# Performance work log

Measured on AMD Instinct MI355X. Metric: run time of the kernel, lower is better.

Reference implementation:

```python
import jax, jax.numpy as jnp
import numpy as np

S, B, D, H, F, E = 2048, 2, 768, 12, 3072, 8
DH = D // H
T = S * B
CAP = int(2.0 * T / E)  # capacity factor 2.0


def layer_norm(x, g, b, eps=1e-5):
    m = jnp.mean(x, axis=-1, keepdims=True)
    v = jnp.var(x, axis=-1, keepdims=True)
    return (x - m) * jax.lax.rsqrt(v + eps) * g + b


def setup_inputs() -> dict:
    key = jax.random.key(0)
    ks = jax.random.split(key, 16)
    sc = 0.02
    return {
        "src": jax.random.normal(ks[0], (S, B, D), jnp.float32),
        "in_proj_w": sc * jax.random.normal(ks[1], (3 * D, D), jnp.float32),
        "in_proj_b": sc * jax.random.normal(ks[2], (3 * D,), jnp.float32),
        "out_proj_w": sc * jax.random.normal(ks[3], (D, D), jnp.float32),
        "out_proj_b": sc * jax.random.normal(ks[4], (D,), jnp.float32),
        "norm1_g": 1.0 + sc * jax.random.normal(ks[5], (D,), jnp.float32),
        "norm1_b": sc * jax.random.normal(ks[6], (D,), jnp.float32),
        "router_w": sc * jax.random.normal(ks[7], (E, D), jnp.float32),
        "router_b": sc * jax.random.normal(ks[8], (E,), jnp.float32),
        "w1": sc * jax.random.normal(ks[9], (E, D, F), jnp.float32),
        "b1": sc * jax.random.normal(ks[10], (E, F), jnp.float32),
        "w2": sc * jax.random.normal(ks[11], (E, F, D), jnp.float32),
        "b2": sc * jax.random.normal(ks[12], (E, D), jnp.float32),
        "norm2_g": 1.0 + sc * jax.random.normal(ks[13], (D,), jnp.float32),
        "norm2_b": sc * jax.random.normal(ks[14], (D,), jnp.float32),
    }


def reference(src, in_proj_w, in_proj_b, out_proj_w, out_proj_b,
              norm1_g, norm1_b, router_w, router_b, w1, b1, w2, b2,
              norm2_g, norm2_b):
    # ---- multi-head self-attention (dropout = identity, eval mode) ----
    qkv = src @ in_proj_w.T + in_proj_b                # [S,B,3D]
    q, k, v = jnp.split(qkv, 3, axis=-1)

    def heads(t):  # [S,B,D] -> [B,H,S,DH]
        return t.reshape(S, B, H, DH).transpose(1, 2, 0, 3)

    q, k, v = heads(q), heads(k), heads(v)
    scores = jnp.einsum('bhsd,bhtd->bhst', q, k) / np.float32(np.sqrt(DH))
    attn = jax.nn.softmax(scores, axis=-1)
    ctx = jnp.einsum('bhst,bhtd->bhsd', attn, v)       # [B,H,S,DH]
    ctx = ctx.transpose(2, 0, 1, 3).reshape(S, B, D)
    attn_out = ctx @ out_proj_w.T + out_proj_b

    x = layer_norm(src + attn_out, norm1_g, norm1_b)

    # ---- Switch MoE FFN: top-1 routing, capacity-based dispatch ----
    tok = x.reshape(T, D)
    logits = tok @ router_w.T + router_b               # [T,E]
    probs = jax.nn.softmax(logits, axis=-1)
    eidx = jnp.argmax(probs, axis=-1)                  # [T]
    gate = jnp.take_along_axis(probs, eidx[:, None], axis=-1)[:, 0]
    oh = jax.nn.one_hot(eidx, E, dtype=probs.dtype)    # [T,E]
    # position of each token within its expert's queue
    pos = (jnp.cumsum(oh, axis=0) * oh).sum(-1).astype(jnp.int32) - 1

    # scatter tokens into per-expert buffers (tokens over capacity dropped)
    buf = jnp.zeros((E, CAP, D), tok.dtype).at[eidx, pos].set(tok, mode='drop')
    h = jax.nn.relu(jnp.einsum('ecd,edf->ecf', buf, w1) + b1[:, None, :])
    y = jnp.einsum('ecf,efd->ecd', h, w2) + b2[:, None, :]

    keep = pos < CAP
    out_tok = jnp.where(keep[:, None], y[eidx, jnp.minimum(pos, CAP - 1)], 0.0)
    out_tok = out_tok * gate[:, None]
    moe_out = out_tok.reshape(S, B, D)

    # load-balancing loss: E * sum_e(frac_tokens_e * mean_prob_e)
    f = oh.mean(axis=0)
    P = probs.mean(axis=0)
    lb_loss = E * jnp.sum(f * P)

    out = layer_norm(x + moe_out, norm2_g, norm2_b)
    return (out, lb_loss)
```

## Files before the change

kernel.cpp:

```cpp
#include <hip/hip_runtime.h>
#include <hip/hip_bf16.h>


#define S_   2048
#define B_   2
#define D_   768
#define H_   12
#define DH_  64
#define F_   3072
#define E_   8
#define T_   4096
#define CAP_ 1024

typedef __hip_bfloat16 bf16;
using short8  = __attribute__((ext_vector_type(8))) short;
using floatx4 = __attribute__((ext_vector_type(4))) float;

__device__ __forceinline__ float b2f(bf16 x) { return __bfloat162float(x); }
__device__ __forceinline__ bf16  f2b(float x) { return __float2bfloat16(x); }

struct SrcF32 { const float* p; };
struct SrcPair { const bf16* h; const bf16* l; };

__device__ __forceinline__ void ld_split(const SrcF32& s, size_t off,
                                         short8& hi, short8& lo) {
  const float* q = s.p + off;
  float4 a = *(const float4*)q;
  float4 b = *(const float4*)(q + 4);
  float va[8] = {a.x, a.y, a.z, a.w, b.x, b.y, b.z, b.w};
  __attribute__((aligned(16))) bf16 h[8], l[8];
#pragma unroll
  for (int j = 0; j < 8; j++) {
    bf16 hh = f2b(va[j]);
    h[j] = hh;
    l[j] = f2b(va[j] - b2f(hh));
  }
  hi = *(const short8*)h; lo = *(const short8*)l;
}
__device__ __forceinline__ void ld_split(const SrcPair& s, size_t off,
                                         short8& hi, short8& lo) {
  hi = *(const short8*)(s.h + off);
  lo = *(const short8*)(s.l + off);
}

template <typename SA, typename SW>
__device__ __forceinline__ void gemm_split_loop(
    const SA& A, const SW& W, int K,
    bf16* AsH, bf16* AsL, bf16* WsH, bf16* WsL, floatx4 (&acc)[4][4]) {
  const int tid = threadIdx.x;
  const int w = tid >> 6, lane = tid & 63;
  const int srow = lane >> 2;
  const int scol = (lane & 3) * 8;
  const int r0 = w * 32 + srow;
  const int lds0 = (w * 32 + srow) * 32 + scol;
  const int wm = (w >> 1) * 64, wn = (w & 1) * 64;
  const int fr = lane & 15, g = lane >> 4;

  for (int kt = 0; kt < K; kt += 32) {
    short8 ah0, al0, ah1, al1, wh0, wl0, wh1, wl1;
    ld_split(A, (size_t)r0 * K + kt + scol, ah0, al0);
    ld_split(A, (size_t)(r0 + 16) * K + kt + scol, ah1, al1);
    ld_split(W, (size_t)r0 * K + kt + scol, wh0, wl0);
    ld_split(W, (size_t)(r0 + 16) * K + kt + scol, wh1, wl1);
    __syncthreads();
    *(short8*)(AsH + lds0)       = ah0;
    *(short8*)(AsH + lds0 + 512) = ah1;
    *(short8*)(AsL + lds0)       = al0;
    *(short8*)(AsL + lds0 + 512) = al1;
    *(short8*)(WsH + lds0)       = wh0;
    *(short8*)(WsH + lds0 + 512) = wh1;
    *(short8*)(WsL + lds0)       = wl0;
    *(short8*)(WsL + lds0 + 512) = wl1;
    __syncthreads();
    short8 afh[4], afl[4], bfh[4], bfl[4];
#pragma unroll
    for (int mi = 0; mi < 4; mi++) {
      int o = (wm + mi * 16 + fr) * 32 + g * 8;
      afh[mi] = *(const short8*)&AsH[o];
      afl[mi] = *(const short8*)&AsL[o];
    }
#pragma unroll
    for (int ni = 0; ni < 4; ni++) {
      int o = (wn + ni * 16 + fr) * 32 + g * 8;
      bfh[ni] = *(const short8*)&WsH[o];
      bfl[ni] = *(const short8*)&WsL[o];
    }
#pragma unroll
    for (int mi = 0; mi < 4; mi++)
#pragma unroll
      for (int ni = 0; ni < 4; ni++) {
        floatx4 z = acc[mi][ni];
        z = __builtin_amdgcn_mfma_f32_16x16x32_bf16(afh[mi], bfh[ni], z, 0, 0, 0);
        z = __builtin_amdgcn_mfma_f32_16x16x32_bf16(afh[mi], bfl[ni], z, 0, 0, 0);
        z = __builtin_amdgcn_mfma_f32_16x16x32_bf16(afl[mi], bfh[ni], z, 0, 0, 0);
        acc[mi][ni] = z;
      }
  }
}

template <typename SA, typename SW>
__global__ __launch_bounds__(256) void gemm_split_pairout(
    SA A, SW W, const float* __restrict__ bias,
    bf16* __restrict__ Chi, bf16* __restrict__ Clo, int N, int K,
    int m_base, int n_base) {
  __shared__ __attribute__((aligned(16))) bf16 AsH[4096], AsL[4096];
  __shared__ __attribute__((aligned(16))) bf16 WsH[4096], WsL[4096];
  const int m0 = m_base + blockIdx.y * 128, n0 = n_base + blockIdx.x * 128;
  SA Ab = A; SW Wb = W;
  Ab.p ? (void)0 : (void)0;
  floatx4 acc[4][4];
#pragma unroll
  for (int i = 0; i < 4; i++)
#pragma unroll
    for (int j = 0; j < 4; j++) acc[i][j] = (floatx4){0.f, 0.f, 0.f, 0.f};
  SA As2 = A;
  SA Aoff = A; Aoff.p = A.p + (size_t)m0 * K;
  SW Woff = W; Woff.p = W.p + (size_t)n0 * K;
  gemm_split_loop(Aoff, Woff, K, AsH, AsL, WsH, WsL, acc);

  const int tid = threadIdx.x, w = tid >> 6, lane = tid & 63;
  const int wm = (w >> 1) * 64, wn = (w & 1) * 64;
  const int fr = lane & 15, rg = (lane >> 4) * 4;
#pragma unroll
  for (int mi = 0; mi < 4; mi++) {
#pragma unroll
    for (int ni = 0; ni < 4; ni++) {
      int n = n0 + wn + ni * 16 + fr;
      float bv = bias[n];
#pragma unroll
      for (int r = 0; r < 4; r++) {
        int m = m0 + wm + mi * 16 + rg + r;
        float v = acc[mi][ni][r] + bv;
        bf16 hh = f2b(v);
        Chi[(size_t)m * N + n] = hh;
        Clo[(size_t)m * N + n] = f2b(v - b2f(hh));
      }
    }
  }
}

template <typename SA>
__global__ __launch_bounds__(256) void gemm_split_f32out(
    SA A, SrcF32 W, const float* __restrict__ bias,
    const float* __restrict__ resid, float* __restrict__ C, int N, int K) {
  __shared__ __attribute__((aligned(16))) bf16 AsH[4096], AsL[4096];
  __shared__ __attribute__((aligned(16))) bf16 WsH[4096], WsL[4096];
  const int m0 = blockIdx.y * 128, n0 = blockIdx.x * 128;
  floatx4 acc[4][4];
#pragma unroll
  for (int i = 0; i < 4; i++)
#pragma unroll
    for (int j = 0; j < 4; j++) acc[i][j] = (floatx4){0.f, 0.f, 0.f, 0.f};
  SA Aoff = A; Aoff.h = A.h + (size_t)m0 * K; Aoff.l = A.l + (size_t)m0 * K;
  SrcF32 Woff; Woff.p = W.p + (size_t)n0 * K;
  gemm_split_loop(Aoff, Woff, K, AsH, AsL, WsH, WsL, acc);

  const int tid = threadIdx.x, w = tid >> 6, lane = tid & 63;
  const int wm = (w >> 1) * 64, wn = (w & 1) * 64;
  const int fr = lane & 15, rg = (lane >> 4) * 4;
#pragma unroll
  for (int mi = 0; mi < 4; mi++) {
#pragma unroll
    for (int ni = 0; ni < 4; ni++) {
      int n = n0 + wn + ni * 16 + fr;
      float bv = bias[n];
#pragma unroll
      for (int r = 0; r < 4; r++) {
        int m = m0 + wm + mi * 16 + rg + r;
        C[(size_t)m * N + n] = acc[mi][ni][r] + bv + resid[(size_t)m * N + n];
      }
    }
  }
}

__device__ __forceinline__ void gemm_tile_loop(
    const bf16* __restrict__ Ablk, const bf16* __restrict__ Wblk, int K,
    bf16* As, bf16* Ws, floatx4 (&acc)[4][4]) {
  const int tid = threadIdx.x;
  const int w = tid >> 6, lane = tid & 63;
  const int srow = lane >> 2;
  const int scol = (lane & 3) * 8;
  const bf16* Ag = Ablk + (size_t)(w * 32 + srow) * K + scol;
  const bf16* Wg = Wblk + (size_t)(w * 32 + srow) * K + scol;
  bf16* AsW = As + (w * 32 + srow) * 32 + scol;
  bf16* WsW = Ws + (w * 32 + srow) * 32 + scol;
  const int wm = (w >> 1) * 64, wn = (w & 1) * 64;
  const int fr = lane & 15, g = lane >> 4;

  for (int kt = 0; kt < K; kt += 32) {
    short8 a0 = *(const short8*)(Ag);
    short8 a1 = *(const short8*)(Ag + 16 * (size_t)K);
    short8 w0 = *(const short8*)(Wg);
    short8 w1v = *(const short8*)(Wg + 16 * (size_t)K);
    Ag += 32; Wg += 32;
    __syncthreads();
    *(short8*)(AsW)           = a0;
    *(short8*)(AsW + 16 * 32) = a1;
    *(short8*)(WsW)           = w0;
    *(short8*)(WsW + 16 * 32) = w1v;
    __syncthreads();
    short8 af[4], bfg[4];
#pragma unroll
    for (int mi = 0; mi < 4; mi++)
      af[mi] = *(const short8*)&As[(wm + mi * 16 + fr) * 32 + g * 8];
#pragma unroll
    for (int ni = 0; ni < 4; ni++)
      bfg[ni] = *(const short8*)&Ws[(wn + ni * 16 + fr) * 32 + g * 8];
#pragma unroll
    for (int mi = 0; mi < 4; mi++)
#pragma unroll
      for (int ni = 0; ni < 4; ni++)
        acc[mi][ni] = __builtin_amdgcn_mfma_f32_16x16x32_bf16(
            af[mi], bfg[ni], acc[mi][ni], 0, 0, 0);
  }
}

__global__ __launch_bounds__(256) void moe1_kernel(
    const bf16* __restrict__ xe, const bf16* __restrict__ w1t,
    const float* __restrict__ b1, bf16* __restrict__ h,
    const int* __restrict__ counts) {
  const int e = blockIdx.y >> 3, lt = blockIdx.y & 7;
  int kept = counts[e]; if (kept > CAP_) kept = CAP_;
  if (lt * 128 >= kept) return;
  __shared__ __attribute__((aligned(16))) bf16 As[4096];
  __shared__ __attribute__((aligned(16))) bf16 Ws[4096];
  const int n0 = blockIdx.x * 128;
  floatx4 acc[4][4];
#pragma unroll
  for (int i = 0; i < 4; i++)
#pragma unroll
    for (int j = 0; j < 4; j++) acc[i][j] = (floatx4){0.f, 0.f, 0.f, 0.f};
  gemm_tile_loop(xe + (size_t)(e * CAP_ + lt * 128) * D_,
                 w1t + (size_t)e * F_ * D_ + (size_t)n0 * D_, D_, As, Ws, acc);

  const int tid = threadIdx.x, w = tid >> 6, lane = tid & 63;
  const int wm = (w >> 1) * 64, wn = (w & 1) * 64;
  const int fr = lane & 15, rg = (lane >> 4) * 4;
#pragma unroll
  for (int mi = 0; mi < 4; mi++) {
#pragma unroll
    for (int ni = 0; ni < 4; ni++) {
      int n = n0 + wn + ni * 16 + fr;
      float bv = b1[e * F_ + n];
#pragma unroll
      for (int r = 0; r < 4; r++) {
        int mrow = lt * 128 + wm + mi * 16 + rg + r;
        h[(size_t)(e * CAP_ + mrow) * F_ + n] =
            f2b(fmaxf(acc[mi][ni][r] + bv, 0.f));
      }
    }
  }
}

__global__ __launch_bounds__(256) void moe2_kernel(
    const bf16* __restrict__ h, const bf16* __restrict__ w2t,
    const float* __restrict__ bias2, const int* __restrict__ stok,
    const float* __restrict__ sgate, const int* __restrict__ counts,
    bf16* __restrict__ moe) {
  const int e = blockIdx.y >> 3, lt = blockIdx.y & 7;
  int kept = counts[e]; if (kept > CAP_) kept = CAP_;
  if (lt * 128 >= kept) return;
  __shared__ __attribute__((aligned(16))) bf16 As[4096];
  __shared__ __attribute__((aligned(16))) bf16 Ws[4096];
  const int n0 = blockIdx.x * 128;
  floatx4 acc[4][4];
#pragma unroll
  for (int i = 0; i < 4; i++)
#pragma unroll
    for (int j = 0; j < 4; j++) acc[i][j] = (floatx4){0.f, 0.f, 0.f, 0.f};
  gemm_tile_loop(h + (size_t)(e * CAP_ + lt * 128) * F_,
                 w2t + (size_t)e * D_ * F_ + (size_t)n0 * F_, F_, As, Ws, acc);

  const int tid = threadIdx.x, w = tid >> 6, lane = tid & 63;
  const int wm = (w >> 1) * 64, wn = (w & 1) * 64;
  const int fr = lane & 15, rg = (lane >> 4) * 4;
#pragma unroll
  for (int mi = 0; mi < 4; mi++) {
#pragma unroll
    for (int r = 0; r < 4; r++) {
      int mrow = lt * 128 + wm + mi * 16 + rg + r;
      int slot = e * CAP_ + mrow;
      int t = stok[slot];
      if (t < 0) continue;
      float gt = sgate[slot];
#pragma unroll
      for (int ni = 0; ni < 4; ni++) {
        int n = n0 + wn + ni * 16 + fr;
        moe[(size_t)t * D_ + n] = f2b((acc[mi][ni][r] + bias2[e * D_ + n]) * gt);
      }
    }
  }
}

__global__ __launch_bounds__(256) void attn_kernel(
    const bf16* __restrict__ qh, const bf16* __restrict__ ql,
    bf16* __restrict__ ch, bf16* __restrict__ cl) {
  __shared__ __attribute__((aligned(16))) bf16 KsH[64 * 72], KsL[64 * 72];
  __shared__ __attribute__((aligned(16))) bf16 VsH[64 * 72], VsL[64 * 72];
  __shared__ __attribute__((aligned(16))) bf16 PsH[4][16 * 72], PsL[4][16 * 72];
  const int tid = threadIdx.x, w = tid >> 6, lane = tid & 63;
  const int bh = blockIdx.y, b = bh / H_, hh = bh % H_;
  const int q0 = blockIdx.x * 64;
  const int fr = lane & 15, g = lane >> 4;

  const int qs = q0 + w * 16 + fr;
  const size_t qoff = (size_t)(qs * B_ + b) * (3 * D_) + hh * DH_;
  const short8 qf0h = *(const short8*)(qh + qoff + g * 8);
  const short8 qf1h = *(const short8*)(qh + qoff + 32 + g * 8);
  const short8 qf0l = *(const short8*)(ql + qoff + g * 8);
  const short8 qf1l = *(const short8*)(ql + qoff + 32 + g * 8);

  float mi_[4], li_[4], alpha[4];
  floatx4 o[4];
#pragma unroll
  for (int r = 0; r < 4; r++) { mi_[r] = -1e30f; li_[r] = 0.f; }
#pragma unroll
  for (int nt = 0; nt < 4; nt++) o[nt] = (floatx4){0.f, 0.f, 0.f, 0.f};

  const int str = tid >> 2;
  const int st16 = (tid & 3) * 16;

  for (int kb = 0; kb < S_ / 64; kb++) {
    const int s0 = kb * 64;
    __syncthreads();
    {
      const size_t koff = (size_t)((s0 + str) * B_ + b) * (3 * D_) + D_ +
                          hh * DH_ + st16;
      *(short8*)&KsH[str * 72 + st16]     = *(const short8*)(qh + koff);
      *(short8*)&KsH[str * 72 + st16 + 8] = *(const short8*)(qh + koff + 8);
      *(short8*)&KsL[str * 72 + st16]     = *(const short8*)(ql + koff);
      *(short8*)&KsL[str * 72 + st16 + 8] = *(const short8*)(ql + koff + 8);
    }
    {
      const size_t voff = (size_t)((s0 + str) * B_ + b) * (3 * D_) + 2 * D_ +
                          hh * DH_ + st16;
      short8 a0 = *(const short8*)(qh + voff);
      short8 a1 = *(const short8*)(qh + voff + 8);
      short8 c0 = *(const short8*)(ql + voff);
      short8 c1 = *(const short8*)(ql + voff + 8);
      const bf16* p0 = (const bf16*)&a0;
      const bf16* p1 = (const bf16*)&a1;
      const bf16* p2 = (const bf16*)&c0;
      const bf16* p3 = (const bf16*)&c1;
#pragma unroll
      for (int j = 0; j < 8; j++) {
        VsH[(st16 + j) * 72 + str]     = p0[j];
        VsH[(st16 + 8 + j) * 72 + str] = p1[j];
        VsL[(st16 + j) * 72 + str]     = p2[j];
        VsL[(st16 + 8 + j) * 72 + str] = p3[j];
      }
    }
    __syncthreads();

    floatx4 sc[4];
#pragma unroll
    for (int nt = 0; nt < 4; nt++) {
      int krow = nt * 16 + fr;
      short8 k0h = *(const short8*)&KsH[krow * 72 + g * 8];
      short8 k1h = *(const short8*)&KsH[krow * 72 + 32 + g * 8];
      short8 k0l = *(const short8*)&KsL[krow * 72 + g * 8];
      short8 k1l = *(const short8*)&KsL[krow * 72 + 32 + g * 8];
      floatx4 z = (floatx4){0.f, 0.f, 0.f, 0.f};
      z = __builtin_amdgcn_mfma_f32_16x16x32_bf16(qf0h, k0h, z, 0, 0, 0);
      z = __builtin_amdgcn_mfma_f32_16x16x32_bf16(qf1h, k1h, z, 0, 0, 0);
      z = __builtin_amdgcn_mfma_f32_16x16x32_bf16(qf0h, k0l, z, 0, 0, 0);
      z = __builtin_amdgcn_mfma_f32_16x16x32_bf16(qf1h, k1l, z, 0, 0, 0);
      z = __builtin_amdgcn_mfma_f32_16x16x32_bf16(qf0l, k0h, z, 0, 0, 0);
      z = __builtin_amdgcn_mfma_f32_16x16x32_bf16(qf1l, k1h, z, 0, 0, 0);
      sc[nt] = z;
    }
#pragma unroll
    for (int nt = 0; nt < 4; nt++)
#pragma unroll
      for (int r = 0; r < 4; r++) sc[nt][r] *= 0.125f;

#pragma unroll
    for (int r = 0; r < 4; r++) {
      float mx = fmaxf(fmaxf(sc[0][r], sc[1][r]), fmaxf(sc[2][r], sc[3][r]));
#pragma unroll
      for (int d = 1; d < 16; d <<= 1) mx = fmaxf(mx, __shfl_xor(mx, d));
      float mn = fmaxf(mi_[r], mx);
      alpha[r] = __expf(mi_[r] - mn);
      float rs = 0.f;
#pragma unroll
      for (int nt = 0; nt < 4; nt++) {
        float p = __expf(sc[nt][r] - mn);
        sc[nt][r] = p; rs += p;
      }
#pragma unroll
      for (int d = 1; d < 16; d <<= 1) rs += __shfl_xor(rs, d);
      li_[r] = li_[r] * alpha[r] + rs;
      mi_[r] = mn;
    }
#pragma unroll
    for (int nt = 0; nt < 4; nt++)
#pragma unroll
      for (int r = 0; r < 4; r++) o[nt][r] *= alpha[r];

    bf16* PwH = &PsH[w][0];
    bf16* PwL = &PsL[w][0];
#pragma unroll
    for (int nt = 0; nt < 4; nt++)
#pragma unroll
      for (int r = 0; r < 4; r++) {
        float p = sc[nt][r];
        bf16 hh2 = f2b(p);
        PwH[((g << 2) + r) * 72 + nt * 16 + fr] = hh2;
        PwL[((g << 2) + r) * 72 + nt * 16 + fr] = f2b(p - b2f(hh2));
      }
    __syncthreads();

    short8 p0h = *(const short8*)&PwH[fr * 72 + g * 8];
    short8 p1h = *(const short8*)&PwH[fr * 72 + 32 + g * 8];
    short8 p0l = *(const short8*)&PwL[fr * 72 + g * 8];
    short8 p1l = *(const short8*)&PwL[fr * 72 + 32 + g * 8];
#pragma unroll
    for (int nt = 0; nt < 4; nt++) {
      int dh = nt * 16 + fr;
      short8 v0h = *(const short8*)&VsH[dh * 72 + g * 8];
      short8 v1h = *(const short8*)&VsH[dh * 72 + 32 + g * 8];
      short8 v0l = *(const short8*)&VsL[dh * 72 + g * 8];
      short8 v1l = *(const short8*)&VsL[dh * 72 + 32 + g * 8];
      floatx4 z = o[nt];
      z = __builtin_amdgcn_mfma_f32_16x16x32_bf16(p0h, v0h, z, 0, 0, 0);
      z = __builtin_amdgcn_mfma_f32_16x16x32_bf16(p1h, v1h, z, 0, 0, 0);
      z = __builtin_amdgcn_mfma_f32_16x16x32_bf16(p0h, v0l, z, 0, 0, 0);
      z = __builtin_amdgcn_mfma_f32_16x16x32_bf16(p1h, v1l, z, 0, 0, 0);
      z = __builtin_amdgcn_mfma_f32_16x16x32_bf16(p0l, v0h, z, 0, 0, 0);
      z = __builtin_amdgcn_mfma_f32_16x16x32_bf16(p1l, v1h, z, 0, 0, 0);
      o[nt] = z;
    }
  }

#pragma unroll
  for (int nt = 0; nt < 4; nt++) {
#pragma unroll
    for (int r = 0; r < 4; r++) {
      int qrow = q0 + w * 16 + (g << 2) + r;
      float li = fmaxf(li_[r], 1e-20f);
      float v = o[nt][r] / li;
      size_t off = (size_t)(qrow * B_ + b) * D_ + hh * DH_ + nt * 16 + fr;
      bf16 hh2 = f2b(v);
      ch[off] = hh2;
      cl[off] = f2b(v - b2f(hh2));
    }
  }
}

__global__ __launch_bounds__(256) void transpose_kernel(
    const float* __restrict__ src, bf16* __restrict__ dst, int R, int C) {
  __shared__ bf16 tile[64][65];
  const int tid = threadIdx.x;
  const size_t boff = (size_t)blockIdx.z * R * C;
  const int c0 = blockIdx.x * 64, r0 = blockIdx.y * 64;
#pragma unroll
  for (int i = 0; i < 2; i++) {
    int rr = i * 32 + tid / 8, cc = (tid % 8) * 8;
    const float* sp = &src[boff + (size_t)(r0 + rr) * C + c0 + cc];
    float4 v0 = *(const float4*)sp;
    float4 v1 = *(const float4*)(sp + 4);
    tile[rr][cc + 0] = f2b(v0.x); tile[rr][cc + 1] = f2b(v0.y);
    tile[rr][cc + 2] = f2b(v0.z); tile[rr][cc + 3] = f2b(v0.w);
    tile[rr][cc + 4] = f2b(v1.x); tile[rr][cc + 5] = f2b(v1.y);
    tile[rr][cc + 6] = f2b(v1.z); tile[rr][cc + 7] = f2b(v1.w);
  }
  __syncthreads();
#pragma unroll
  for (int i = 0; i < 2; i++) {
    int cc = i * 32 + tid / 8, rr = (tid % 8) * 8;
    __attribute__((aligned(16))) bf16 tmp[8];
#pragma unroll
    for (int j = 0; j < 8; j++) tmp[j] = tile[rr + j][cc];
    *(short8*)&dst[boff + (size_t)(c0 + cc) * R + r0 + rr] =
        *(const short8*)tmp;
  }
}

__global__ __launch_bounds__(256) void ln_kernel(
    const float* __restrict__ x, const bf16* __restrict__ add,
    const float* __restrict__ gam, const float* __restrict__ bet,
    float* __restrict__ out) {
  const int row = blockIdx.x, tid = threadIdx.x;
  float v[3], s = 0.f, sq = 0.f;
#pragma unroll
  for (int j = 0; j < 3; j++) {
    int c = tid + j * 256;
    float t = x[(size_t)row * D_ + c];
    if (add) t += b2f(add[(size_t)row * D_ + c]);
    v[j] = t; s += t; sq += t * t;
  }
#pragma unroll
  for (int d = 1; d < 64; d <<= 1) { s += __shfl_xor(s, d); sq += __shfl_xor(sq, d); }
  __shared__ float ss[4], ssq[4];
  const int w = tid >> 6, lane = tid & 63;
  if (lane == 0) { ss[w] = s; ssq[w] = sq; }
  __syncthreads();
  s = ss[0] + ss[1] + ss[2] + ss[3];
  sq = ssq[0] + ssq[1] + ssq[2] + ssq[3];
  float mean = s * (1.f / D_);
  float var = fmaxf(sq * (1.f / D_) - mean * mean, 0.f);
  float rstd = rsqrtf(var + 1e-5f);
#pragma unroll
  for (int j = 0; j < 3; j++) {
    int c = tid + j * 256;
    out[(size_t)row * D_ + c] = (v[j] - mean) * rstd * gam[c] + bet[c];
  }
}

__global__ __launch_bounds__(256) void router_kernel(
    const float* __restrict__ x, const float* __restrict__ rw,
    const float* __restrict__ rb, float* __restrict__ probs,
    int* __restrict__ eidx, float* __restrict__ gate) {
  const int tid = threadIdx.x, w = tid >> 6, lane = tid & 63;
  const int t = blockIdx.x * 4 + w;
  float acc[E_];
#pragma unroll
  for (int e = 0; e < E_; e++) acc[e] = 0.f;
  for (int j = 0; j < D_ / 64; j++) {
    int c = lane + j * 64;
    float xv = x[(size_t)t * D_ + c];
#pragma unroll
    for (int e = 0; e < E_; e++) acc[e] += xv * rw[e * D_ + c];
  }
#pragma unroll
  for (int e = 0; e < E_; e++)
#pragma unroll
    for (int d = 1; d < 64; d <<= 1) acc[e] += __shfl_xor(acc[e], d);
  if (lane == 0) {
    float lg[E_], p[E_], mx = -1e30f;
#pragma unroll
    for (int e = 0; e < E_; e++) { lg[e] = acc[e] + rb[e]; mx = fmaxf(mx, lg[e]); }
    float sum = 0.f;
#pragma unroll
    for (int e = 0; e < E_; e++) { p[e] = __expf(lg[e] - mx); sum += p[e]; }
    float inv = 1.f / sum;
    int am = 0; float bm = lg[0];
#pragma unroll
    for (int e = 1; e < E_; e++) if (lg[e] > bm) { bm = lg[e]; am = e; }
#pragma unroll
    for (int e = 0; e < E_; e++) probs[t * E_ + e] = p[e] * inv;
    eidx[t] = am;
    gate[t] = p[am] * inv;
  }
}

__global__ __launch_bounds__(512) void router_pos_kernel(
    const int* __restrict__ eidx, const float* __restrict__ probs,
    const float* __restrict__ gate, int* __restrict__ stok,
    float* __restrict__ sgate, int* __restrict__ counts,
    float* __restrict__ lb_out) {
  const int tid = threadIdx.x, e = tid >> 6, lane = tid & 63;
  int base = 0; float sump = 0.f;
  for (int c = 0; c < T_ / 64; c++) {
    int t = c * 64 + lane;
    int ei = eidx[t];
    sump += probs[t * E_ + e];
    bool m = (ei == e);
    unsigned long long mask = __ballot(m);
    if (m) {
      int p = base + (int)__popcll(mask & ((1ull << lane) - 1ull));
      if (p < CAP_) {
        stok[e * CAP_ + p] = t;
        sgate[e * CAP_ + p] = gate[t];
      }
    }
    base += (int)__popcll(mask);
  }
#pragma unroll
  for (int d = 1; d < 64; d <<= 1) sump += __shfl_xor(sump, d);
  __shared__ float sP[E_];
  __shared__ int sC[E_];
  if (lane == 0) { counts[e] = base; sC[e] = base; sP[e] = sump; }
  __syncthreads();
  if (tid == 0) {
    float lb = 0.f;
    for (int i = 0; i < E_; i++) lb += (float)sC[i] * sP[i];
    lb *= (float)E_ / ((float)T_ * (float)T_);
    lb_out[0] = lb;
  }
}

__global__ __launch_bounds__(256) void gather_kernel(
    const float* __restrict__ x, const int* __restrict__ stok,
    bf16* __restrict__ xe) {
  int idx = blockIdx.x * 256 + threadIdx.x;
  int slot = idx / (D_ / 4), r = idx % (D_ / 4);
  int t = stok[slot];
  bf16 o0, o1, o2, o3;
  if (t >= 0) {
    float4 v = *(const float4*)(x + (size_t)t * D_ + r * 4);
    o0 = f2b(v.x); o1 = f2b(v.y); o2 = f2b(v.z); o3 = f2b(v.w);
  } else {
    o0 = o1 = o2 = o3 = f2b(0.f);
  }
  bf16* dst = xe + (size_t)slot * D_ + r * 4;
  dst[0] = o0; dst[1] = o1; dst[2] = o2; dst[3] = o3;
}

extern "C" void kernel_launch(void* const* d_in, const int* in_sizes, int n_in,
                              void* d_out, int out_size, void* d_ws,
                              size_t ws_size, hipStream_t stream) {
  const float* src   = (const float*)d_in[0];
  const float* in_w  = (const float*)d_in[1];
  const float* in_b  = (const float*)d_in[2];
  const float* out_w = (const float*)d_in[3];
  const float* out_b = (const float*)d_in[4];
  const float* n1g   = (const float*)d_in[5];
  const float* n1b   = (const float*)d_in[6];
  const float* rw    = (const float*)d_in[7];
  const float* rb    = (const float*)d_in[8];
  const float* w1    = (const float*)d_in[9];
  const float* b1    = (const float*)d_in[10];
  const float* w2    = (const float*)d_in[11];
  const float* b2p   = (const float*)d_in[12];
  const float* n2g   = (const float*)d_in[13];
  const float* n2b   = (const float*)d_in[14];
  float* out = (float*)d_out;

  char* ws = (char*)d_ws;
  bf16*  qkv_h  = (bf16*)(ws + 0);
  bf16*  qkv_l  = (bf16*)(ws + 18874368);
  bf16*  w1t    = (bf16*)(ws + 0);
  bf16*  w2t    = (bf16*)(ws + 0);
  bf16*  ctx_h  = (bf16*)(ws + 37748736);
  bf16*  ctx_l  = (bf16*)(ws + 44040192);
  bf16*  xe     = (bf16*)(ws + 37748736);
  bf16*  moe    = (bf16*)(ws + 37748736);
  float* xln    = (float*)(ws + 50331648);
  bf16*  hbuf   = (bf16*)(ws + 62914560);
  float* probs  = (float*)(ws + 113246208);
  int*   eidx   = (int*)(ws + 113377280);
  float* gate   = (float*)(ws + 113393664);
  int*   counts = (int*)(ws + 113410048);
  int*   stok   = (int*)(ws + 113410304);
  float* sgate  = (float*)(ws + 113443072);

  (void)in_sizes; (void)n_in; (void)out_size; (void)ws_size;

  hipMemsetAsync(stok, 0xFF, E_ * CAP_ * sizeof(int), stream);

  gemm_split_pairout<SrcF32, SrcF32>
      <<<dim3(3 * D_ / 128, T_ / 128), 256, 0, stream>>>(
          SrcF32{src}, SrcF32{in_w}, in_b, qkv_h, qkv_l, 3 * D_, D_, 0, 0);
  attn_kernel<<<dim3(S_ / 64, B_ * H_), 256, 0, stream>>>(
      qkv_h, qkv_l, ctx_h, ctx_l);
  gemm_split_f32out<SrcPair>
      <<<dim3(D_ / 128, T_ / 128), 256, 0, stream>>>(
          SrcPair{ctx_h, ctx_l}, SrcF32{out_w}, out_b, src, xln, D_, D_);
  ln_kernel<<<T_, 256, 0, stream>>>(xln, nullptr, n1g, n1b, xln);
  router_kernel<<<T_ / 4, 256, 0, stream>>>(xln, rw, rb, probs, eidx, gate);
  router_pos_kernel<<<1, 512, 0, stream>>>(eidx, probs, gate, stok, sgate,
                                           counts, out + (size_t)T_ * D_);
  gather_kernel<<<(E_ * CAP_ * (D_ / 4)) / 256, 256, 0, stream>>>(xln, stok, xe);
  transpose_kernel<<<dim3(F_ / 64, D_ / 64, E_), 256, 0, stream>>>(w1, w1t, D_, F_);
  moe1_kernel<<<dim3(F_ / 128, E_ * (CAP_ / 128)), 256, 0, stream>>>(
      xe, w1t, b1, hbuf, counts);
  hipMemsetAsync(moe, 0, (size_t)T_ * D_ * sizeof(bf16), stream);
  transpose_kernel<<<dim3(D_ / 64, F_ / 64, E_), 256, 0, stream>>>(w2, w2t, F_, D_);
  moe2_kernel<<<dim3(D_ / 128, E_ * (CAP_ / 128)), 256, 0, stream>>>(
      hbuf, w2t, b2p, stok, sgate, counts, moe);
  ln_kernel<<<T_, 256, 0, stream>>>(xln, moe, n2g, n2b, out);
}
```

Before: 737.4 us.

## Pre-transpose V into a global buffer and pad attention LDS rows

```diff
diff --git a/kernel.cpp b/kernel.cpp
--- a/kernel.cpp
+++ b/kernel.cpp
@@ -11,6 +11,8 @@
 #define E_   8
 #define T_   4096
 #define CAP_ 1024
+
+#define AP_  68
 
 typedef __hip_bfloat16 bf16;
 using short8  = __attribute__((ext_vector_type(8))) short;
@@ -98,24 +100,19 @@
   }
 }
 
-template <typename SA, typename SW>
 __global__ __launch_bounds__(256) void gemm_split_pairout(
-    SA A, SW W, const float* __restrict__ bias,
-    bf16* __restrict__ Chi, bf16* __restrict__ Clo, int N, int K,
-    int m_base, int n_base) {
+    SrcF32 A, SrcF32 W, const float* __restrict__ bias,
+    bf16* __restrict__ Chi, bf16* __restrict__ Clo, int N, int K) {
   __shared__ __attribute__((aligned(16))) bf16 AsH[4096], AsL[4096];
   __shared__ __attribute__((aligned(16))) bf16 WsH[4096], WsL[4096];
-  const int m0 = m_base + blockIdx.y * 128, n0 = n_base + blockIdx.x * 128;
-  SA Ab = A; SW Wb = W;
-  Ab.p ? (void)0 : (void)0;
+  const int m0 = blockIdx.y * 128, n0 = blockIdx.x * 128;
   floatx4 acc[4][4];
 #pragma unroll
   for (int i = 0; i < 4; i++)
 #pragma unroll
     for (int j = 0; j < 4; j++) acc[i][j] = (floatx4){0.f, 0.f, 0.f, 0.f};
-  SA As2 = A;
-  SA Aoff = A; Aoff.p = A.p + (size_t)m0 * K;
-  SW Woff = W; Woff.p = W.p + (size_t)n0 * K;
+  SrcF32 Aoff{A.p + (size_t)m0 * K};
+  SrcF32 Woff{W.p + (size_t)n0 * K};
   gemm_split_loop(Aoff, Woff, K, AsH, AsL, WsH, WsL, acc);
 
   const int tid = threadIdx.x, w = tid >> 6, lane = tid & 63;
@@ -139,9 +136,8 @@
   }
 }
 
-template <typename SA>
 __global__ __launch_bounds__(256) void gemm_split_f32out(
-    SA A, SrcF32 W, const float* __restrict__ bias,
+    SrcPair A, SrcF32 W, const float* __restrict__ bias,
     const float* __restrict__ resid, float* __restrict__ C, int N, int K) {
   __shared__ __attribute__((aligned(16))) bf16 AsH[4096], AsL[4096];
   __shared__ __attribute__((aligned(16))) bf16 WsH[4096], WsL[4096];
@@ -151,8 +147,8 @@
   for (int i = 0; i < 4; i++)
 #pragma unroll
     for (int j = 0; j < 4; j++) acc[i][j] = (floatx4){0.f, 0.f, 0.f, 0.f};
-  SA Aoff = A; Aoff.h = A.h + (size_t)m0 * K; Aoff.l = A.l + (size_t)m0 * K;
-  SrcF32 Woff; Woff.p = W.p + (size_t)n0 * K;
+  SrcPair Aoff{A.h + (size_t)m0 * K, A.l + (size_t)m0 * K};
+  SrcF32 Woff{W.p + (size_t)n0 * K};
   gemm_split_loop(Aoff, Woff, K, AsH, AsL, WsH, WsL, acc);
 
   const int tid = threadIdx.x, w = tid >> 6, lane = tid & 63;
@@ -292,12 +288,44 @@
   }
 }
 
+__global__ __launch_bounds__(256) void vtrans2_kernel(
+    const bf16* __restrict__ qh, const bf16* __restrict__ ql,
+    bf16* __restrict__ vth, bf16* __restrict__ vtl) {
+  __shared__ bf16 th[64][65], tl[64][65];
+  const int tid = threadIdx.x;
+  const int bh = blockIdx.y, b = bh / H_, hh = bh % H_;
+  const int s0 = blockIdx.x * 64;
+#pragma unroll
+  for (int i = 0; i < 2; i++) {
+    int rr = i * 32 + tid / 8, cc = (tid % 8) * 8;
+    size_t off = (size_t)((s0 + rr) * B_ + b) * (3 * D_) + 2 * D_ + hh * DH_ + cc;
+    short8 vh = *(const short8*)(qh + off);
+    short8 vl = *(const short8*)(ql + off);
+    const bf16* ph = (const bf16*)&vh;
+    const bf16* pl = (const bf16*)&vl;
+#pragma unroll
+    for (int j = 0; j < 8; j++) { th[rr][cc + j] = ph[j]; tl[rr][cc + j] = pl[j]; }
+  }
+  __syncthreads();
+#pragma unroll
+  for (int i = 0; i < 2; i++) {
+    int cc = i * 32 + tid / 8, rr = (tid % 8) * 8;
+    __attribute__((aligned(16))) bf16 a[8], c[8];
+#pragma unroll
+    for (int j = 0; j < 8; j++) { a[j] = th[rr + j][cc]; c[j] = tl[rr + j][cc]; }
+    size_t off = ((size_t)bh * DH_ + cc) * S_ + s0 + rr;
+    *(short8*)(vth + off) = *(const short8*)a;
+    *(short8*)(vtl + off) = *(const short8*)c;
+  }
+}
+
 __global__ __launch_bounds__(256) void attn_kernel(
     const bf16* __restrict__ qh, const bf16* __restrict__ ql,
+    const bf16* __restrict__ vth, const bf16* __restrict__ vtl,
     bf16* __restrict__ ch, bf16* __restrict__ cl) {
-  __shared__ __attribute__((aligned(16))) bf16 KsH[64 * 72], KsL[64 * 72];
-  __shared__ __attribute__((aligned(16))) bf16 VsH[64 * 72], VsL[64 * 72];
-  __shared__ __attribute__((aligned(16))) bf16 PsH[4][16 * 72], PsL[4][16 * 72];
+  __shared__ __attribute__((aligned(16))) bf16 KsH[64 * AP_], KsL[64 * AP_];
+  __shared__ __attribute__((aligned(16))) bf16 VsH[64 * AP_], VsL[64 * AP_];
+  __shared__ __attribute__((aligned(16))) bf16 PsH[4][16 * AP_], PsL[4][16 * AP_];
   const int tid = threadIdx.x, w = tid >> 6, lane = tid & 63;
   const int bh = blockIdx.y, b = bh / H_, hh = bh % H_;
   const int q0 = blockIdx.x * 64;
@@ -326,29 +354,17 @@
     {
       const size_t koff = (size_t)((s0 + str) * B_ + b) * (3 * D_) + D_ +
                           hh * DH_ + st16;
-      *(short8*)&KsH[str * 72 + st16]     = *(const short8*)(qh + koff);
-      *(short8*)&KsH[str * 72 + st16 + 8] = *(const short8*)(qh + koff + 8);
-      *(short8*)&KsL[str * 72 + st16]     = *(const short8*)(ql + koff);
-      *(short8*)&KsL[str * 72 + st16 + 8] = *(const short8*)(ql + koff + 8);
+      *(short8*)&KsH[str * AP_ + st16]     = *(const short8*)(qh + koff);
+      *(short8*)&KsH[str * AP_ + st16 + 8] = *(const short8*)(qh + koff + 8);
+      *(short8*)&KsL[str * AP_ + st16]     = *(const short8*)(ql + koff);
+      *(short8*)&KsL[str * AP_ + st16 + 8] = *(const short8*)(ql + koff + 8);
     }
     {
-      const size_t voff = (size_t)((s0 + str) * B_ + b) * (3 * D_) + 2 * D_ +
-                          hh * DH_ + st16;
-      short8 a0 = *(const short8*)(qh + voff);
-      short8 a1 = *(const short8*)(qh + voff + 8);
-      short8 c0 = *(const short8*)(ql + voff);
-      short8 c1 = *(const short8*)(ql + voff + 8);
-      const bf16* p0 = (const bf16*)&a0;
-      const bf16* p1 = (const bf16*)&a1;
-      const bf16* p2 = (const bf16*)&c0;
-      const bf16* p3 = (const bf16*)&c1;
-#pragma unroll
-      for (int j = 0; j < 8; j++) {
-        VsH[(st16 + j) * 72 + str]     = p0[j];
-        VsH[(st16 + 8 + j) * 72 + str] = p1[j];
-        VsL[(st16 + j) * 72 + str]     = p2[j];
-        VsL[(st16 + 8 + j) * 72 + str] = p3[j];
-      }
+      const size_t voff = ((size_t)bh * DH_ + str) * S_ + s0 + st16;
+      *(short8*)&VsH[str * AP_ + st16]     = *(const short8*)(vth + voff);
+      *(short8*)&VsH[str * AP_ + st16 + 8] = *(const short8*)(vth + voff + 8);
+      *(short8*)&VsL[str * AP_ + st16]     = *(const short8*)(vtl + voff);
+      *(short8*)&VsL[str * AP_ + st16 + 8] = *(const short8*)(vtl + voff + 8);
     }
     __syncthreads();
 
@@ -356,10 +372,10 @@
 #pragma unroll
     for (int nt = 0; nt < 4; nt++) {
       int krow = nt * 16 + fr;
-      short8 k0h = *(const short8*)&KsH[krow * 72 + g * 8];
-      short8 k1h = *(const short8*)&KsH[krow * 72 + 32 + g * 8];
-      short8 k0l = *(const short8*)&KsL[krow * 72 + g * 8];
-      short8 k1l = *(const short8*)&KsL[krow * 72 + 32 + g * 8];
+      short8 k0h = *(const short8*)&KsH[krow * AP_ + g * 8];
+      short8 k1h = *(const short8*)&KsH[krow * AP_ + 32 + g * 8];
+      short8 k0l = *(const short8*)&KsL[krow * AP_ + g * 8];
+      short8 k1l = *(const short8*)&KsL[krow * AP_ + 32 + g * 8];
       floatx4 z = (floatx4){0.f, 0.f, 0.f, 0.f};
       z = __builtin_amdgcn_mfma_f32_16x16x32_bf16(qf0h, k0h, z, 0, 0, 0);
       z = __builtin_amdgcn_mfma_f32_16x16x32_bf16(qf1h, k1h, z, 0, 0, 0);
@@ -405,22 +421,22 @@
       for (int r = 0; r < 4; r++) {
         float p = sc[nt][r];
         bf16 hh2 = f2b(p);
-        PwH[((g << 2) + r) * 72 + nt * 16 + fr] = hh2;
-        PwL[((g << 2) + r) * 72 + nt * 16 + fr] = f2b(p - b2f(hh2));
+        PwH[((g << 2) + r) * AP_ + nt * 16 + fr] = hh2;
+        PwL[((g << 2) + r) * AP_ + nt * 16 + fr] = f2b(p - b2f(hh2));
       }
     __syncthreads();
 
-    short8 p0h = *(const short8*)&PwH[fr * 72 + g * 8];
-    short8 p1h = *(const short8*)&PwH[fr * 72 + 32 + g * 8];
-    short8 p0l = *(const short8*)&PwL[fr * 72 + g * 8];
-    short8 p1l = *(const short8*)&PwL[fr * 72 + 32 + g * 8];
+    short8 p0h = *(const short8*)&PwH[fr * AP_ + g * 8];
+    short8 p1h = *(const short8*)&PwH[fr * AP_ + 32 + g * 8];
+    short8 p0l = *(const short8*)&PwL[fr * AP_ + g * 8];
+    short8 p1l = *(const short8*)&PwL[fr * AP_ + 32 + g * 8];
 #pragma unroll
     for (int nt = 0; nt < 4; nt++) {
       int dh = nt * 16 + fr;
-      short8 v0h = *(const short8*)&VsH[dh * 72 + g * 8];
-      short8 v1h = *(const short8*)&VsH[dh * 72 + 32 + g * 8];
-      short8 v0l = *(const short8*)&VsL[dh * 72 + g * 8];
-      short8 v1l = *(const short8*)&VsL[dh * 72 + 32 + g * 8];
+      short8 v0h = *(const short8*)&VsH[dh * AP_ + g * 8];
+      short8 v1h = *(const short8*)&VsH[dh * AP_ + 32 + g * 8];
+      short8 v0l = *(const short8*)&VsL[dh * AP_ + g * 8];
+      short8 v1l = *(const short8*)&VsL[dh * AP_ + 32 + g * 8];
       floatx4 z = o[nt];
       z = __builtin_amdgcn_mfma_f32_16x16x32_bf16(p0h, v0h, z, 0, 0, 0);
       z = __builtin_amdgcn_mfma_f32_16x16x32_bf16(p1h, v1h, z, 0, 0, 0);
@@ -627,6 +643,8 @@
   bf16*  xe     = (bf16*)(ws + 37748736);
   bf16*  moe    = (bf16*)(ws + 37748736);
   float* xln    = (float*)(ws + 50331648);
+  bf16*  vt_h   = (bf16*)(ws + 62914560);
+  bf16*  vt_l   = (bf16*)(ws + 69206016);
   bf16*  hbuf   = (bf16*)(ws + 62914560);
   float* probs  = (float*)(ws + 113246208);
   int*   eidx   = (int*)(ws + 113377280);
@@ -639,14 +657,14 @@
 
   hipMemsetAsync(stok, 0xFF, E_ * CAP_ * sizeof(int), stream);
 
-  gemm_split_pairout<SrcF32, SrcF32>
-      <<<dim3(3 * D_ / 128, T_ / 128), 256, 0, stream>>>(
-          SrcF32{src}, SrcF32{in_w}, in_b, qkv_h, qkv_l, 3 * D_, D_, 0, 0);
+  gemm_split_pairout<<<dim3(3 * D_ / 128, T_ / 128), 256, 0, stream>>>(
+      SrcF32{src}, SrcF32{in_w}, in_b, qkv_h, qkv_l, 3 * D_, D_);
+  vtrans2_kernel<<<dim3(S_ / 64, B_ * H_), 256, 0, stream>>>(
+      qkv_h, qkv_l, vt_h, vt_l);
   attn_kernel<<<dim3(S_ / 64, B_ * H_), 256, 0, stream>>>(
-      qkv_h, qkv_l, ctx_h, ctx_l);
-  gemm_split_f32out<SrcPair>
-      <<<dim3(D_ / 128, T_ / 128), 256, 0, stream>>>(
-          SrcPair{ctx_h, ctx_l}, SrcF32{out_w}, out_b, src, xln, D_, D_);
+      qkv_h, qkv_l, vt_h, vt_l, ctx_h, ctx_l);
+  gemm_split_f32out<<<dim3(D_ / 128, T_ / 128), 256, 0, stream>>>(
+      SrcPair{ctx_h, ctx_l}, SrcF32{out_w}, out_b, src, xln, D_, D_);
   ln_kernel<<<T_, 256, 0, stream>>>(xln, nullptr, n1g, n1b, xln);
   router_kernel<<<T_ / 4, 256, 0, stream>>>(xln, rw, rb, probs, eidx, gate);
   router_pos_kernel<<<1, 512, 0, stream>>>(eidx, probs, gate, stok, sgate,
```

After: 734.5 us. Within noise of the previous version (-0.4%).
